# Performance work log

Measured on AMD Instinct MI355X. Metric: run time of the kernel, lower is better.

Reference implementation:

```python
import jax, jax.numpy as jnp
import numpy as np

N_NODES = 16384
N_EDGES = 131072
EDGE_DIM = 16
IN_CH = 32
OUT_CH = 32
HID_EDGE = 64
MLP_HID = 64  # int(32 * 2.0)
OUT_FINAL = 10
N_GRAPHS = 64
BN_EPS = 1e-5


def setup_inputs() -> dict:
    key = jax.random.key(0)
    ks = jax.random.split(key, 20)
    s = lambda *sh: 1.0 / np.sqrt(sh[0])
    inp = {
        'x': jax.random.normal(ks[0], (N_NODES, IN_CH), jnp.float32),
        'edge_attr': jax.random.normal(ks[1], (N_EDGES, EDGE_DIM), jnp.float32),
        'edge_index': jax.random.randint(ks[2], (2, N_EDGES), 0, N_NODES, jnp.int64),
        'batch': jnp.sort(jax.random.randint(ks[3], (N_NODES,), 0, N_GRAPHS, jnp.int64)),
    }
    # layer 0: edge MLP (EDGE_DIM->HID_EDGE->IN_CH*OUT_CH), root, bias, BN affine
    inp['w1_0'] = jax.random.normal(ks[4], (EDGE_DIM, HID_EDGE), jnp.float32) * s(EDGE_DIM)
    inp['b1_0'] = jnp.zeros((HID_EDGE,), jnp.float32)
    inp['w2_0'] = jax.random.normal(ks[5], (HID_EDGE, IN_CH * OUT_CH), jnp.float32) * s(HID_EDGE)
    inp['b2_0'] = jnp.zeros((IN_CH * OUT_CH,), jnp.float32)
    inp['root_0'] = jax.random.normal(ks[6], (IN_CH, OUT_CH), jnp.float32) * s(IN_CH)
    inp['bias_0'] = jnp.zeros((OUT_CH,), jnp.float32)
    inp['gamma_0'] = jnp.ones((OUT_CH,), jnp.float32)
    inp['beta_0'] = jnp.zeros((OUT_CH,), jnp.float32)
    # layer 1: edge MLP (EDGE_DIM->HID_EDGE->OUT_CH*OUT_CH)
    inp['w1_1'] = jax.random.normal(ks[7], (EDGE_DIM, HID_EDGE), jnp.float32) * s(EDGE_DIM)
    inp['b1_1'] = jnp.zeros((HID_EDGE,), jnp.float32)
    inp['w2_1'] = jax.random.normal(ks[8], (HID_EDGE, OUT_CH * OUT_CH), jnp.float32) * s(HID_EDGE)
    inp['b2_1'] = jnp.zeros((OUT_CH * OUT_CH,), jnp.float32)
    inp['root_1'] = jax.random.normal(ks[9], (OUT_CH, OUT_CH), jnp.float32) * s(OUT_CH)
    inp['bias_1'] = jnp.zeros((OUT_CH,), jnp.float32)
    inp['gamma_1'] = jnp.ones((OUT_CH,), jnp.float32)
    inp['beta_1'] = jnp.zeros((OUT_CH,), jnp.float32)
    # final MLP (dropout is identity in eval / deterministic reference)
    inp['mlp_w1'] = jax.random.normal(ks[10], (OUT_CH, MLP_HID), jnp.float32) * s(OUT_CH)
    inp['mlp_b1'] = jnp.zeros((MLP_HID,), jnp.float32)
    inp['mlp_w2'] = jax.random.normal(ks[11], (MLP_HID, OUT_FINAL), jnp.float32) * s(MLP_HID)
    inp['mlp_b2'] = jnp.zeros((OUT_FINAL,), jnp.float32)
    return inp


def _nnconv(x, src, dst, edge_attr, w1, b1, w2, b2, root, bias, out_ch):
    # per-edge weight matrices from the edge MLP: [E, in, out]
    h = jax.nn.relu(edge_attr @ w1 + b1)
    W = (h @ w2 + b2).reshape(-1, x.shape[1], out_ch)
    msg = jnp.einsum('ei,eio->eo', x[src], W)  # gather + per-edge matmul
    agg = jax.ops.segment_sum(msg, dst, num_segments=N_NODES)
    cnt = jax.ops.segment_sum(jnp.ones((dst.shape[0], 1), x.dtype), dst, num_segments=N_NODES)
    agg = agg / jnp.maximum(cnt, 1.0)  # scatter-mean (zero-degree nodes -> 0)
    return agg + x @ root + bias


def _bn(x, gamma, beta):
    m = jnp.mean(x, axis=0)
    v = jnp.var(x, axis=0)
    return (x - m) * jax.lax.rsqrt(v + BN_EPS) * gamma + beta


def reference(x, edge_attr, edge_index, batch,
              w1_0, b1_0, w2_0, b2_0, root_0, bias_0, gamma_0, beta_0,
              w1_1, b1_1, w2_1, b2_1, root_1, bias_1, gamma_1, beta_1,
              mlp_w1, mlp_b1, mlp_w2, mlp_b2):
    src, dst = edge_index[0], edge_index[1]
    h = _nnconv(x, src, dst, edge_attr, w1_0, b1_0, w2_0, b2_0, root_0, bias_0, OUT_CH)
    h = jax.nn.relu(_bn(h, gamma_0, beta_0))
    h = _nnconv(h, src, dst, edge_attr, w1_1, b1_1, w2_1, b2_1, root_1, bias_1, OUT_CH)
    h = jax.nn.relu(_bn(h, gamma_1, beta_1))
    # global mean pool over graphs
    pooled = jax.ops.segment_sum(h, batch, num_segments=N_GRAPHS)
    gcnt = jax.ops.segment_sum(jnp.ones((h.shape[0], 1), h.dtype), batch, num_segments=N_GRAPHS)
    pooled = pooled / jnp.maximum(gcnt, 1.0)
    logits = jax.nn.relu(pooled @ mlp_w1 + mlp_b1) @ mlp_w2 + mlp_b2
    return logits
```

## Files before the change

kernel.cpp:

```cpp
#include <hip/hip_runtime.h>
#include <hip/hip_bf16.h>

#define NN 16384
#define NE 131072
#define NG 64
#define EPB 128

typedef unsigned short u16;
typedef unsigned int u32;
typedef __attribute__((ext_vector_type(8))) short short8;
typedef __attribute__((ext_vector_type(4))) float f32x4;
typedef __attribute__((ext_vector_type(2))) float f32x2;
typedef __attribute__((ext_vector_type(8))) _Float16 f16x8;
typedef __attribute__((ext_vector_type(2))) _Float16 f16x2;
typedef __attribute__((address_space(1))) const unsigned int gu32;
typedef __attribute__((address_space(3))) unsigned int lu32;

__device__ __forceinline__ float bf2f(u16 u) {
    u32 x = ((u32)u) << 16;
    return __builtin_bit_cast(float, x);
}
__device__ __forceinline__ u16 f2bf(float f) {
    u32 u = __builtin_bit_cast(u32, f);
    u = u + 0x7fffu + ((u >> 16) & 1u);
    return (u16)(u >> 16);
}
__device__ __forceinline__ u16 f2h(float f) {
    _Float16 h = (_Float16)f;
    return __builtin_bit_cast(u16, h);
}
__device__ __forceinline__ f16x2 pkrtz(float a, float b) {
    auto v = __builtin_amdgcn_cvt_pkrtz(a, b);
    static_assert(sizeof(v) == 4, "pkrtz size");
    return __builtin_bit_cast(f16x2, v);
}
#if __has_builtin(__builtin_amdgcn_cvt_pk_bf16_f32)
__device__ __forceinline__ u32 pk2bf_fast(float a, float b) {
    auto v = __builtin_amdgcn_cvt_pk_bf16_f32(a, b);
    static_assert(sizeof(v) == 4, "cvt_pk_bf16 size");
    return __builtin_bit_cast(u32, v);
}
#else
__device__ __forceinline__ u32 pk2bf_fast(float a, float b) {
    u32 ua = __builtin_bit_cast(u32, a) + 0x8000u;
    u32 ub = __builtin_bit_cast(u32, b) + 0x8000u;
    return __builtin_amdgcn_perm(ub, ua, 0x07060302u);
}
#endif
__device__ __forceinline__ float loadF(const void* p, int i, bool bf) {
    return bf ? bf2f(((const u16*)p)[i]) : ((const float*)p)[i];
}
__device__ __forceinline__ int loadI(const void* p, int i, bool i64) {
    return i64 ? (int)((const long long*)p)[i] : ((const int*)p)[i];
}
__device__ __forceinline__ bool det_bf(const void* g0) {
    return ((const u16*)g0)[0] == 0x3F80u;
}
__device__ __forceinline__ bool det_i64(const void* eidx) {
    const u32* u = (const u32*)eidx;
    return (u[1] | u[3] | u[5] | u[7]) == 0u;
}

__global__ __launch_bounds__(256) void k_prep(const void* w2a, const void* b2a,
                                              const void* w2b, const void* b2b,
                                              const void* w1a, const void* w1b,
                                              u16* bp0, u16* bp1, u16* w1p0, u16* w1p1,
                                              const void* eidx, float* cnt, u32* eord,
                                              const void* g0) {
    const bool bf = det_bf(g0);
    int id = blockIdx.x * 256 + threadIdx.x;
    if (id < 2 * 66560) {
        int l = id / 66560, v = id % 66560;
        int j = v & 7, lane = (v >> 3) & 63, nt = (v >> 9) & 1, t = v >> 10;
        int kk = (lane >> 4) * 8 + j;
        int n = (lane & 15) + 16 * nt;
        const void* w2 = l ? w2b : w2a;
        const void* b2 = l ? b2b : b2a;
        float val = (t < 64) ? loadF(w2, t * 1024 + kk * 32 + n, bf)
                             : loadF(b2, kk * 32 + n, bf);
        (l ? bp1 : bp0)[v] = f2h(val);
    } else if (id < 2 * 66560 + 2 * 2048) {
        int v = id - 2 * 66560;
        int l = v >> 11; v &= 2047;
        int j = v & 7, lane = (v >> 3) & 63, nt = v >> 9;
        int k = (lane >> 4) * 8 + j;
        int n = nt * 16 + (lane & 15);
        const void* w1 = l ? w1b : w1a;
        float val = (k < 16) ? loadF(w1, k * 64 + n, bf) : 0.f;
        (l ? w1p1 : w1p0)[v] = f2bf(val);
    } else {
        const bool i64 = det_i64(eidx);
        int e = id - (2 * 66560 + 2 * 2048);
        int d = loadI(eidx, NE + e, i64);
        int slot = (int)atomicAdd(&cnt[d], 1.0f);
        if (slot < 64) eord[d * 64 + slot] = (u32)e;
    }
}

__device__ __forceinline__ void stage_chunk(const u16* Bpack, u16* lds, int cc, int w, int lane) {
    const char* src = (const char*)Bpack + (size_t)cc * 8192 + (size_t)(w * 1024 + lane * 16);
    char* dst = (char*)lds + w * 1024;
    __builtin_amdgcn_global_load_lds((gu32*)src, (lu32*)dst, 16, 0, 0);
    __builtin_amdgcn_global_load_lds((gu32*)(src + 4096), (lu32*)(dst + 4096), 16, 0, 0);
}

#define HSTR 72
__global__ __launch_bounds__(256, 4) void k_edge(const void* ea, const u16* w1p, const void* b1,
                                                 const void* xv, int layer1,
                                                 const float* sSp, const float* sQp,
                                                 const void* gammap, const void* betap,
                                                 const void* eidx, const u16* Bpack,
                                                 float* msg, const void* g0) {
    const bool bf = det_bf(g0);
    const bool i64 = det_i64(eidx);
    __shared__ __align__(16) u16 hl[EPB * HSTR];
    __shared__ __align__(16) u16 Bls[2][4096];
    __shared__ __align__(16) float bnS[32], bnB[32];
    const int tid = threadIdx.x;
    const int e0 = blockIdx.x * EPB;
    const int lane = tid & 63;
    const int w = tid >> 6;
    const int q = lane >> 4;
    const int m = lane & 15;
    const int wbl = w * 32;
    const int wb = e0 + wbl;

    stage_chunk(Bpack, Bls[0], 0, w, lane);
    stage_chunk(Bpack, Bls[1], 1, w, lane);

    if (layer1 && tid < 32) {
        float s = 0.f, qq = 0.f;
#pragma unroll
        for (int p = 0; p < 16; p++) { s += sSp[p * 32 + tid]; qq += sQp[p * 32 + tid]; }
        float mn = s * (1.0f / 16384.0f);
        float var = qq * (1.0f / 16384.0f) - mn * mn;
        float inv = rsqrtf(var + 1e-5f);
        float g = loadF(gammap, tid, bf), b = loadF(betap, tid, bf);
        bnS[tid] = inv * g;
        bnB[tid] = b - mn * inv * g;
    }

    {
        short8 Ah[2];
#pragma unroll
        for (int e2 = 0; e2 < 2; e2++) {
            int eg = wb + e2 * 16 + m;
            uint4 av = make_uint4(0u, 0u, 0u, 0u);
            if (bf) {
                uint4 t = *(const uint4*)((const char*)ea + (size_t)eg * 32 + (q & 1) * 16);
                if (q < 2) av = t;
            } else {
                const float4* p = (const float4*)((const char*)ea + (size_t)eg * 64 + (q & 1) * 32);
                float4 a = p[0], b = p[1];
                if (q < 2) av = make_uint4(pk2bf_fast(a.x, a.y), pk2bf_fast(a.z, a.w),
                                           pk2bf_fast(b.x, b.y), pk2bf_fast(b.z, b.w));
            }
            Ah[e2] = __builtin_bit_cast(short8, av);
        }
#pragma unroll
        for (int nt = 0; nt < 4; nt++) {
            uint4 bw = *(const uint4*)&w1p[(nt * 64 + lane) * 8];
            short8 Bf = __builtin_bit_cast(short8, bw);
            float bb = loadF(b1, nt * 16 + m, bf);
#pragma unroll
            for (int e2 = 0; e2 < 2; e2++) {
                f32x4 c = __builtin_amdgcn_mfma_f32_16x16x32_bf16(
                    Ah[e2], Bf, f32x4{0.f, 0.f, 0.f, 0.f}, 0, 0, 0);
                int rbase = (wbl + e2 * 16 + q * 4) * HSTR + nt * 16 + m;
#pragma unroll
                for (int r = 0; r < 4; r++) {
                    _Float16 hv = (_Float16)fmaxf(c[r] + bb, 0.f);
                    hl[rbase + r * HSTR] = __builtin_bit_cast(u16, hv);
                }
            }
        }
    }

    float4 ga[2], gb[2];
#pragma unroll
    for (int mt = 0; mt < 2; mt++) {
        int s = loadI(eidx, wb + mt * 16 + m, i64);
        if (layer1 || !bf) {
            const float4* xp = (const float4*)xv + (size_t)s * 8 + q * 2;
            ga[mt] = xp[0]; gb[mt] = xp[1];
        } else {
            const uint4* xp = (const uint4*)((const char*)xv + (size_t)s * 64 + q * 16);
            uint4 a = *xp;
            ga[mt] = make_float4(bf2f((u16)(a.x & 0xffff)), bf2f((u16)(a.x >> 16)),
                                 bf2f((u16)(a.y & 0xffff)), bf2f((u16)(a.y >> 16)));
            gb[mt] = make_float4(bf2f((u16)(a.z & 0xffff)), bf2f((u16)(a.z >> 16)),
                                 bf2f((u16)(a.w & 0xffff)), bf2f((u16)(a.w >> 16)));
        }
    }

    __syncthreads();

    f16x2 xh[2][4];
    if (layer1) {
        float4 s0 = *(const float4*)&bnS[q * 8], s1 = *(const float4*)&bnS[q * 8 + 4];
        float4 h0 = *(const float4*)&bnB[q * 8], h1 = *(const float4*)&bnB[q * 8 + 4];
#pragma unroll
        for (int mt = 0; mt < 2; mt++) {
            xh[mt][0] = pkrtz(fmaxf(ga[mt].x * s0.x + h0.x, 0.f), fmaxf(ga[mt].y * s0.y + h0.y, 0.f));
            xh[mt][1] = pkrtz(fmaxf(ga[mt].z * s0.z + h0.z, 0.f), fmaxf(ga[mt].w * s0.w + h0.w, 0.f));
            xh[mt][2] = pkrtz(fmaxf(gb[mt].x * s1.x + h1.x, 0.f), fmaxf(gb[mt].y * s1.y + h1.y, 0.f));
            xh[mt][3] = pkrtz(fmaxf(gb[mt].z * s1.z + h1.z, 0.f), fmaxf(gb[mt].w * s1.w + h1.w, 0.f));
        }
    } else {
#pragma unroll
        for (int mt = 0; mt < 2; mt++) {
            xh[mt][0] = pkrtz(ga[mt].x, ga[mt].y);
            xh[mt][1] = pkrtz(ga[mt].z, ga[mt].w);
            xh[mt][2] = pkrtz(gb[mt].x, gb[mt].y);
            xh[mt][3] = pkrtz(gb[mt].z, gb[mt].w);
        }
    }

    f32x4 acc[2][2];
#pragma unroll
    for (int mt = 0; mt < 2; mt++) {
        acc[mt][0] = f32x4{0.f, 0.f, 0.f, 0.f};
        acc[mt][1] = f32x4{0.f, 0.f, 0.f, 0.f};
    }
    int rowb[2];
#pragma unroll
    for (int mt = 0; mt < 2; mt++) rowb[mt] = (wbl + mt * 16 + m) * HSTR;

    for (int cc = 0; cc < 16; cc++) {
        uint2 hw[2];
        hw[0] = *(const uint2*)&hl[rowb[0] + cc * 4];
        hw[1] = *(const uint2*)&hl[rowb[1] + cc * 4];
        const u16* Bb = &Bls[cc & 1][lane * 8];
#pragma unroll
        for (int tt = 0; tt < 4; tt++) {
            uint4 bu0 = *(const uint4*)(Bb + (tt * 2 + 0) * 512);
            uint4 bu1 = *(const uint4*)(Bb + (tt * 2 + 1) * 512);
            f16x8 B0 = __builtin_bit_cast(f16x8, bu0);
            f16x8 B1 = __builtin_bit_cast(f16x8, bu1);
            const u32 sel = (tt & 1) ? 0x03020302u : 0x01000100u;
#pragma unroll
            for (int mt = 0; mt < 2; mt++) {
                u32 wd = (tt & 2) ? hw[mt].y : hw[mt].x;
                u32 hh = __builtin_amdgcn_perm(wd, wd, sel);
                f16x2 h2 = __builtin_bit_cast(f16x2, hh);
                f16x2 p0 = h2 * xh[mt][0];
                f16x2 p1 = h2 * xh[mt][1];
                f16x2 p2 = h2 * xh[mt][2];
                f16x2 p3 = h2 * xh[mt][3];
                uint4 au = make_uint4(__builtin_bit_cast(u32, p0), __builtin_bit_cast(u32, p1),
                                      __builtin_bit_cast(u32, p2), __builtin_bit_cast(u32, p3));
                f16x8 A = __builtin_bit_cast(f16x8, au);
                acc[mt][0] = __builtin_amdgcn_mfma_f32_16x16x32_f16(A, B0, acc[mt][0], 0, 0, 0);
                acc[mt][1] = __builtin_amdgcn_mfma_f32_16x16x32_f16(A, B1, acc[mt][1], 0, 0, 0);
            }
        }
        __syncthreads();
        if (cc < 15) stage_chunk(Bpack, Bls[cc & 1], cc + 2, w, lane);
    }
    {
        const u16* Bb = &Bls[0][lane * 8];
        uint4 bu0 = *(const uint4*)(Bb + 0);
        uint4 bu1 = *(const uint4*)(Bb + 512);
        f16x8 B0 = __builtin_bit_cast(f16x8, bu0);
        f16x8 B1 = __builtin_bit_cast(f16x8, bu1);
#pragma unroll
        for (int mt = 0; mt < 2; mt++) {
            uint4 au = make_uint4(__builtin_bit_cast(u32, xh[mt][0]), __builtin_bit_cast(u32, xh[mt][1]),
                                  __builtin_bit_cast(u32, xh[mt][2]), __builtin_bit_cast(u32, xh[mt][3]));
            f16x8 A = __builtin_bit_cast(f16x8, au);
            acc[mt][0] = __builtin_amdgcn_mfma_f32_16x16x32_f16(A, B0, acc[mt][0], 0, 0, 0);
            acc[mt][1] = __builtin_amdgcn_mfma_f32_16x16x32_f16(A, B1, acc[mt][1], 0, 0, 0);
        }
    }

#pragma unroll
    for (int mt = 0; mt < 2; mt++) {
        float* mp = msg + (size_t)(wb + mt * 16 + q * 4) * 32 + m;
#pragma unroll
        for (int r = 0; r < 4; r++) {
            mp[r * 32] = acc[mt][0][r];
            mp[r * 32 + 16] = acc[mt][1][r];
        }
    }
}

__global__ __launch_bounds__(256) void k_node(const float* msg, const u32* eord, const float* cnt,
                                              const void* xv, int layer1,
                                              const float* sSp, const float* sQp,
                                              const void* gammap, const void* betap,
                                              const void* root, const void* bias,
                                              float* hpre, float* sS, float* sQ,
                                              const void* g0) {
    const bool bf = det_bf(g0);
    const int tid = threadIdx.x;
    const int v = blockIdx.x * 8 + (tid >> 5);
    const int o = tid & 31;
    __shared__ float bnS[32], bnB[32];
    if (layer1) {
        if (tid < 32) {
            float s = 0.f, qq = 0.f;
#pragma unroll
            for (int p = 0; p < 16; p++) { s += sSp[p * 32 + tid]; qq += sQp[p * 32 + tid]; }
            float mn = s * (1.0f / 16384.0f);
            float var = qq * (1.0f / 16384.0f) - mn * mn;
            float inv = rsqrtf(var + 1e-5f);
            float g = loadF(gammap, tid, bf), b = loadF(betap, tid, bf);
            bnS[tid] = inv * g;
            bnB[tid] = b - mn * inv * g;
        }
        __syncthreads();
    }
    float xrow[32];
    if (layer1) {
        const float* x = (const float*)xv + (size_t)v * 32;
#pragma unroll
        for (int i = 0; i < 32; i++) xrow[i] = fmaxf(x[i] * bnS[i] + bnB[i], 0.f);
    } else if (!bf) {
        const float* x = (const float*)xv + (size_t)v * 32;
#pragma unroll
        for (int i = 0; i < 32; i++) xrow[i] = x[i];
    } else {
        const u16* x = (const u16*)xv + (size_t)v * 32;
#pragma unroll
        for (int i = 0; i < 32; i++) xrow[i] = bf2f(x[i]);
    }
    float a;
    if (bf) {
        const u16* R = (const u16*)root;
        a = bf2f(((const u16*)bias)[o]);
#pragma unroll
        for (int i = 0; i < 32; i++) a += xrow[i] * bf2f(R[i * 32 + o]);
    } else {
        const float* R = (const float*)root;
        a = ((const float*)bias)[o];
#pragma unroll
        for (int i = 0; i < 32; i++) a += xrow[i] * R[i * 32 + o];
    }
    int deg = (int)cnt[v];
    if (deg > 64) deg = 64;
    const u32* ep = eord + (size_t)v * 64;
    float av0 = 0.f, av1 = 0.f;
    int j = 0;
    for (; j + 1 < deg; j += 2) {
        u32 ea0 = ep[j], ea1 = ep[j + 1];
        av0 += msg[(size_t)ea0 * 32 + o];
        av1 += msg[(size_t)ea1 * 32 + o];
    }
    if (j < deg) av0 += msg[(size_t)ep[j] * 32 + o];
    float pre = (av0 + av1) / fmaxf(cnt[v], 1.0f) + a;
    hpre[(size_t)v * 32 + o] = pre;

    __shared__ float lS[256], lQ[256];
    lS[tid] = pre;
    lQ[tid] = pre * pre;
    __syncthreads();
#pragma unroll
    for (int off = 128; off >= 32; off >>= 1) {
        if (tid < off) { lS[tid] += lS[tid + off]; lQ[tid] += lQ[tid + off]; }
        __syncthreads();
    }
    if (tid < 32) {
        int slot = (blockIdx.x & 15) * 32 + tid;
        atomicAdd(&sS[slot], lS[tid]);
        atomicAdd(&sQ[slot], lQ[tid]);
    }
}

__global__ __launch_bounds__(256) void k_bnpool(const float* hpre, const float* sS, const float* sQ,
                                                const void* gamma, const void* beta,
                                                const void* batch, float* pooled, float* gcnt,
                                                const void* eidx, const void* g0) {
    const bool bf = det_bf(g0);
    const bool i64 = det_i64(eidx);
    const int tid = threadIdx.x;
    const int o = tid & 31;
    const int c = tid >> 5;
    float s = 0.f, qq = 0.f;
#pragma unroll
    for (int p = 0; p < 16; p++) { s += sS[p * 32 + o]; qq += sQ[p * 32 + o]; }
    float mn = s * (1.0f / 16384.0f);
    float var = qq * (1.0f / 16384.0f) - mn * mn;
    float inv = rsqrtf(var + 1e-5f);
    float gg = loadF(gamma, o, bf), bb = loadF(beta, o, bf);

    const int base = blockIdx.x * 256 + c;
    float acc = 0.f, cacc = 0.f;
    int curg = -1;
#pragma unroll 4
    for (int j = 0; j < 32; j++) {
        int v = base + j * 8;
        int g = loadI(batch, v, i64);
        float y = fmaxf((hpre[(size_t)v * 32 + o] - mn) * inv * gg + bb, 0.f);
        if (g != curg) {
            if (curg >= 0) {
                atomicAdd(&pooled[curg * 32 + o], acc);
                if (o == 0) atomicAdd(&gcnt[curg], cacc);
            }
            acc = 0.f; cacc = 0.f; curg = g;
        }
        acc += y; cacc += 1.f;
    }
    if (curg >= 0) {
        atomicAdd(&pooled[curg * 32 + o], acc);
        if (o == 0) atomicAdd(&gcnt[curg], cacc);
    }
}

__global__ __launch_bounds__(64) void k_final(const float* pooled, const float* gcnt,
                        const void* w1, const void* b1, const void* w2, const void* b2,
                        void* out, const void* g0) {
    const bool bf = det_bf(g0);
    const int g = blockIdx.x;
    const int j = threadIdx.x;
    float inv = 1.0f / fmaxf(gcnt[g], 1.0f);
    float a = loadF(b1, j, bf);
#pragma unroll
    for (int i = 0; i < 32; i++) {
        float p = pooled[g * 32 + i] * inv;
        a += p * loadF(w1, i * 64 + j, bf);
    }
    a = fmaxf(a, 0.f);
    float lg[10];
#pragma unroll
    for (int c = 0; c < 10; c++) lg[c] = a * loadF(w2, j * 10 + c, bf);
#pragma unroll
    for (int off = 32; off >= 1; off >>= 1) {
#pragma unroll
        for (int c = 0; c < 10; c++) lg[c] += __shfl_down(lg[c], off, 64);
    }
    if (j == 0) {
        if (bf) {
            u16* op = (u16*)out;
#pragma unroll
            for (int c = 0; c < 10; c++) op[g * 10 + c] = f2bf(lg[c] + loadF(b2, c, bf));
        } else {
            float* op = (float*)out;
#pragma unroll
            for (int c = 0; c < 10; c++) op[g * 10 + c] = lg[c] + loadF(b2, c, bf);
        }
    }
}

extern "C" void kernel_launch(void* const* d_in, const int* in_sizes, int n_in,
                              void* d_out, int out_size, void* d_ws, size_t ws_size,
                              hipStream_t stream) {
    char* ws = (char*)d_ws;
    u16* bp0  = (u16*)(ws + 256);
    u16* bp1  = (u16*)(ws + 256 + 133120);
    u16* w1p0 = (u16*)(ws + 266496);
    u16* w1p1 = (u16*)(ws + 270592);
    char* zbase = ws + 274688;
    float* cnt    = (float*)(zbase);
    float* sS0    = (float*)(zbase + 65536);
    float* sQ0    = (float*)(zbase + 67584);
    float* sS1    = (float*)(zbase + 69632);
    float* sQ1    = (float*)(zbase + 71680);
    float* pooled = (float*)(zbase + 73728);
    float* gcnt   = (float*)(zbase + 81920);
    const size_t zsize = 82176;
    char* nz = zbase + 82176;
    u32*   eord  = (u32*)(nz);
    float* msg   = (float*)(nz + 4194304);
    float* hpre0 = (float*)(nz + 4194304 + 16777216);
    float* hpre1 = (float*)(nz + 4194304 + 16777216 + 2097152);

    const void* x     = d_in[0];
    const void* ea    = d_in[1];
    const void* eidx  = d_in[2];
    const void* batch = d_in[3];
    const void* g0    = d_in[10];

    (void)hipMemsetAsync(zbase, 0, zsize, stream);
    k_prep<<<1048, 256, 0, stream>>>(d_in[6], d_in[7], d_in[14], d_in[15],
                                     d_in[4], d_in[12],
                                     bp0, bp1, w1p0, w1p1, eidx, cnt, eord, g0);

    k_edge<<<NE / EPB, 256, 0, stream>>>(ea, w1p0, d_in[5], x, 0,
                                         nullptr, nullptr, nullptr, nullptr,
                                         eidx, bp0, msg, g0);
    k_node<<<NN / 8, 256, 0, stream>>>(msg, eord, cnt, x, 0,
                                       nullptr, nullptr, nullptr, nullptr,
                                       d_in[8], d_in[9], hpre0, sS0, sQ0, g0);

    k_edge<<<NE / EPB, 256, 0, stream>>>(ea, w1p1, d_in[13], hpre0, 1,
                                         sS0, sQ0, d_in[10], d_in[11],
                                         eidx, bp1, msg, g0);
    k_node<<<NN / 8, 256, 0, stream>>>(msg, eord, cnt, hpre0, 1,
                                       sS0, sQ0, d_in[10], d_in[11],
                                       d_in[16], d_in[17], hpre1, sS1, sQ1, g0);

    k_bnpool<<<NN / 256, 256, 0, stream>>>(hpre1, sS1, sQ1, d_in[18], d_in[19], batch,
                                           pooled, gcnt, eidx, g0);
    k_final<<<NG, 64, 0, stream>>>(pooled, gcnt, d_in[20], d_in[21], d_in[22], d_in[23], d_out, g0);
}
```

Measured before the change: 209.8 us.

## Fuse BN-pool and final MLP into one per-graph kernel; vectorize node row loads

Replaces the atomic-based BN+pool kernel and the separate final MLP kernel with a single kernel that runs one block per graph. Each block finds its node range by binary search on the sorted batch array, reduces in shared memory and applies the MLP directly. This removes a launch, the global atomics and part of the memset. It assumes batch is sorted and runs only 64 blocks. Node-row loads in the node kernel are also switched to float4.

```diff
diff --git a/kernel.cpp b/kernel.cpp
--- a/kernel.cpp
+++ b/kernel.cpp
@@ -10,7 +10,6 @@
 typedef unsigned int u32;
 typedef __attribute__((ext_vector_type(8))) short short8;
 typedef __attribute__((ext_vector_type(4))) float f32x4;
-typedef __attribute__((ext_vector_type(2))) float f32x2;
 typedef __attribute__((ext_vector_type(8))) _Float16 f16x8;
 typedef __attribute__((ext_vector_type(2))) _Float16 f16x2;
 typedef __attribute__((address_space(1))) const unsigned int gu32;
@@ -312,13 +311,21 @@
     }
     float xrow[32];
     if (layer1) {
-        const float* x = (const float*)xv + (size_t)v * 32;
-#pragma unroll
-        for (int i = 0; i < 32; i++) xrow[i] = fmaxf(x[i] * bnS[i] + bnB[i], 0.f);
+        const float4* x4 = (const float4*)((const float*)xv + (size_t)v * 32);
+        float4 xa[8];
+#pragma unroll
+        for (int i = 0; i < 8; i++) xa[i] = x4[i];
+        const float* xs = (const float*)xa;
+#pragma unroll
+        for (int i = 0; i < 32; i++) xrow[i] = fmaxf(xs[i] * bnS[i] + bnB[i], 0.f);
     } else if (!bf) {
-        const float* x = (const float*)xv + (size_t)v * 32;
-#pragma unroll
-        for (int i = 0; i < 32; i++) xrow[i] = x[i];
+        const float4* x4 = (const float4*)((const float*)xv + (size_t)v * 32);
+        float4 xa[8];
+#pragma unroll
+        for (int i = 0; i < 8; i++) xa[i] = x4[i];
+        const float* xs = (const float*)xa;
+#pragma unroll
+        for (int i = 0; i < 32; i++) xrow[i] = xs[i];
     } else {
         const u16* x = (const u16*)xv + (size_t)v * 32;
 #pragma unroll
@@ -366,77 +373,77 @@
     }
 }
 
-__global__ __launch_bounds__(256) void k_bnpool(const float* hpre, const float* sS, const float* sQ,
-                                                const void* gamma, const void* beta,
-                                                const void* batch, float* pooled, float* gcnt,
-                                                const void* eidx, const void* g0) {
+__global__ __launch_bounds__(256) void k_tail(const float* hpre, const float* sS, const float* sQ,
+                                              const void* gamma, const void* beta,
+                                              const void* batch,
+                                              const void* w1, const void* b1,
+                                              const void* w2, const void* b2,
+                                              void* out, const void* eidx, const void* g0) {
     const bool bf = det_bf(g0);
     const bool i64 = det_i64(eidx);
+    const int g = blockIdx.x;
     const int tid = threadIdx.x;
     const int o = tid & 31;
     const int c = tid >> 5;
+    __shared__ float lS[256];
+    __shared__ float pool[32];
+
     float s = 0.f, qq = 0.f;
 #pragma unroll
-    for (int p = 0; p < 16; p++) { s += sS[p * 32 + o]; qq += sQ[p * 32 + o]; }
+    for (int pp = 0; pp < 16; pp++) { s += sS[pp * 32 + o]; qq += sQ[pp * 32 + o]; }
     float mn = s * (1.0f / 16384.0f);
     float var = qq * (1.0f / 16384.0f) - mn * mn;
     float inv = rsqrtf(var + 1e-5f);
     float gg = loadF(gamma, o, bf), bb = loadF(beta, o, bf);
 
-    const int base = blockIdx.x * 256 + c;
-    float acc = 0.f, cacc = 0.f;
-    int curg = -1;
-#pragma unroll 4
-    for (int j = 0; j < 32; j++) {
-        int v = base + j * 8;
-        int g = loadI(batch, v, i64);
-        float y = fmaxf((hpre[(size_t)v * 32 + o] - mn) * inv * gg + bb, 0.f);
-        if (g != curg) {
-            if (curg >= 0) {
-                atomicAdd(&pooled[curg * 32 + o], acc);
-                if (o == 0) atomicAdd(&gcnt[curg], cacc);
+    int lo = 0, hi = NN;
+    while (lo < hi) {
+        int mid = (lo + hi) >> 1;
+        if (loadI(batch, mid, i64) < g) lo = mid + 1; else hi = mid;
+    }
+    int lo2 = lo, hi2 = NN;
+    while (lo2 < hi2) {
+        int mid = (lo2 + hi2) >> 1;
+        if (loadI(batch, mid, i64) < g + 1) lo2 = mid + 1; else hi2 = mid;
+    }
+    const int nbeg = lo, nend = lo2;
+
+    float acc = 0.f;
+    for (int v = nbeg + c; v < nend; v += 8)
+        acc += fmaxf((hpre[(size_t)v * 32 + o] - mn) * inv * gg + bb, 0.f);
+    lS[tid] = acc;
+    __syncthreads();
+#pragma unroll
+    for (int off = 4; off >= 1; off >>= 1) {
+        if (c < off) lS[tid] += lS[tid + off * 32];
+        __syncthreads();
+    }
+    if (tid < 32) pool[o] = lS[o] / fmaxf((float)(nend - nbeg), 1.0f);
+    __syncthreads();
+
+    if (tid < 64) {
+        float a = loadF(b1, tid, bf);
+#pragma unroll
+        for (int i = 0; i < 32; i++) a += pool[i] * loadF(w1, i * 64 + tid, bf);
+        a = fmaxf(a, 0.f);
+        float lg[10];
+#pragma unroll
+        for (int cc = 0; cc < 10; cc++) lg[cc] = a * loadF(w2, tid * 10 + cc, bf);
+#pragma unroll
+        for (int off = 32; off >= 1; off >>= 1) {
+#pragma unroll
+            for (int cc = 0; cc < 10; cc++) lg[cc] += __shfl_down(lg[cc], off, 64);
+        }
+        if (tid == 0) {
+            if (bf) {
+                u16* op = (u16*)out;
+#pragma unroll
+                for (int cc = 0; cc < 10; cc++) op[g * 10 + cc] = f2bf(lg[cc] + loadF(b2, cc, bf));
+            } else {
+                float* op = (float*)out;
+#pragma unroll
+                for (int cc = 0; cc < 10; cc++) op[g * 10 + cc] = lg[cc] + loadF(b2, cc, bf);
             }
-            acc = 0.f; cacc = 0.f; curg = g;
-        }
-        acc += y; cacc += 1.f;
-    }
-    if (curg >= 0) {
-        atomicAdd(&pooled[curg * 32 + o], acc);
-        if (o == 0) atomicAdd(&gcnt[curg], cacc);
-    }
-}
-
-__global__ __launch_bounds__(64) void k_final(const float* pooled, const float* gcnt,
-                        const void* w1, const void* b1, const void* w2, const void* b2,
-                        void* out, const void* g0) {
-    const bool bf = det_bf(g0);
-    const int g = blockIdx.x;
-    const int j = threadIdx.x;
-    float inv = 1.0f / fmaxf(gcnt[g], 1.0f);
-    float a = loadF(b1, j, bf);
-#pragma unroll
-    for (int i = 0; i < 32; i++) {
-        float p = pooled[g * 32 + i] * inv;
-        a += p * loadF(w1, i * 64 + j, bf);
-    }
-    a = fmaxf(a, 0.f);
-    float lg[10];
-#pragma unroll
-    for (int c = 0; c < 10; c++) lg[c] = a * loadF(w2, j * 10 + c, bf);
-#pragma unroll
-    for (int off = 32; off >= 1; off >>= 1) {
-#pragma unroll
-        for (int c = 0; c < 10; c++) lg[c] += __shfl_down(lg[c], off, 64);
-    }
-    if (j == 0) {
-        if (bf) {
-            u16* op = (u16*)out;
-#pragma unroll
-            for (int c = 0; c < 10; c++) op[g * 10 + c] = f2bf(lg[c] + loadF(b2, c, bf));
-        } else {
-            float* op = (float*)out;
-#pragma unroll
-            for (int c = 0; c < 10; c++) op[g * 10 + c] = lg[c] + loadF(b2, c, bf);
         }
     }
 }
@@ -455,9 +462,7 @@
     float* sQ0    = (float*)(zbase + 67584);
     float* sS1    = (float*)(zbase + 69632);
     float* sQ1    = (float*)(zbase + 71680);
-    float* pooled = (float*)(zbase + 73728);
-    float* gcnt   = (float*)(zbase + 81920);
-    const size_t zsize = 82176;
+    const size_t zsize = 73728;
     char* nz = zbase + 82176;
     u32*   eord  = (u32*)(nz);
     float* msg   = (float*)(nz + 4194304);
@@ -489,7 +494,6 @@
                                        sS0, sQ0, d_in[10], d_in[11],
                                        d_in[16], d_in[17], hpre1, sS1, sQ1, g0);
 
-    k_bnpool<<<NN / 256, 256, 0, stream>>>(hpre1, sS1, sQ1, d_in[18], d_in[19], batch,
-                                           pooled, gcnt, eidx, g0);
-    k_final<<<NG, 64, 0, stream>>>(pooled, gcnt, d_in[20], d_in[21], d_in[22], d_in[23], d_out, g0);
-}
+    k_tail<<<NG, 256, 0, stream>>>(hpre1, sS1, sQ1, d_in[18], d_in[19], batch,
+                                   d_in[20], d_in[21], d_in[22], d_in[23], d_out, eidx, g0);
+}
```

Measured after the change: 211.8 us. Within noise of the previous version (+1.0%).
